# Optimization experiments

Hardware: AMD Instinct MI355X
Metric: run time of the kernel (lower is better)

The kernel has to match this reference:

```python
import jax, jax.numpy as jnp
import numpy as np

H = 56; W = 56; WS = 7; SHIFT = 3; C = 128; NH = 4; HD = C // NH
N = WS * WS; NW = (H // WS) * (W // WS); B = 64; HID = 4 * C
ALPHA = (1, 2, 4, 8); SCALE = HD ** -0.5


def _rel_index_np():
    coords = np.stack(np.meshgrid(np.arange(WS), np.arange(WS), indexing="ij"))
    cf = coords.reshape(2, -1)
    rel = (cf[:, :, None] - cf[:, None, :]).transpose(1, 2, 0).copy()
    rel[:, :, 0] += WS - 1
    rel[:, :, 1] += WS - 1
    rel[:, :, 0] *= 2 * WS - 1
    return rel.sum(-1).astype(np.int32)  # (N, N)


def _attn_mask_np():
    img = np.zeros((1, H, W, 1), np.float32)
    cnt = 0
    sl = (slice(0, -WS), slice(-WS, -SHIFT), slice(-SHIFT, None))
    for hs in sl:
        for ws in sl:
            img[:, hs, ws, :] = cnt
            cnt += 1
    mw = img.reshape(1, H // WS, WS, W // WS, WS, 1).transpose(0, 1, 3, 2, 4, 5).reshape(-1, N)
    am = mw[:, None, :] - mw[:, :, None]
    return np.where(am != 0, -100.0, 0.0).astype(np.float32)  # (NW, N, N)


def setup_inputs() -> dict:
    key = jax.random.key(0)
    ks = jax.random.split(key, 8)
    p = lambda k, shp, s=0.02: jax.random.normal(k, shp, jnp.float32) * s
    return {
        "x": jax.random.normal(ks[0], (B, H * W, C), jnp.float32),
        "gumbel_weights": jax.nn.softmax(jax.random.normal(ks[1], (4,), jnp.float32)),
        "norm1_w": jnp.ones((C,), jnp.float32), "norm1_b": jnp.zeros((C,), jnp.float32),
        "qkv_w": p(ks[2], (3 * C, C)), "qkv_b": jnp.zeros((3 * C,), jnp.float32),
        "rel_bias_table": p(ks[3], ((2 * WS - 1) ** 2, NH)),
        "proj_w": p(ks[4], (C, C)), "proj_b": jnp.zeros((C,), jnp.float32),
        "attn_mask": jnp.asarray(_attn_mask_np()),
        "norm2_w": jnp.ones((C,), jnp.float32), "norm2_b": jnp.zeros((C,), jnp.float32),
        "fc1_w": p(ks[5], (HID, C)), "fc1_b": jnp.zeros((HID,), jnp.float32),
        "fc2_w": p(ks[6], (C, HID)), "fc2_b": jnp.zeros((C,), jnp.float32),
        "rel_index": jnp.asarray(_rel_index_np()),
    }


def _ln(x, w, b, eps=1e-5):
    mu = x.mean(-1, keepdims=True)
    var = ((x - mu) ** 2).mean(-1, keepdims=True)
    return (x - mu) * jax.lax.rsqrt(var + eps) * w + b


def _win_part(x):  # (B,H,W,C) -> (B*NW, N, C)
    b = x.shape[0]
    x = x.reshape(b, H // WS, WS, W // WS, WS, C).transpose(0, 1, 3, 2, 4, 5)
    return x.reshape(-1, N, C)


def _win_rev(w, b):  # (b*NW, N, C) -> (b,H,W,C)
    x = w.reshape(b, H // WS, W // WS, WS, WS, C).transpose(0, 1, 3, 2, 4, 5)
    return x.reshape(b, H, W, C)


def _window_attn(xw, qkv_w, qkv_b, bias, mask, proj_w, proj_b):
    b = xw.shape[0]
    qkv = (xw @ qkv_w.T + qkv_b).reshape(b, N, 3, NH, HD).transpose(2, 0, 3, 1, 4)
    q, k, v = qkv[0] * SCALE, qkv[1], qkv[2]  # (b,NH,N,HD)
    a = jnp.einsum("bhnd,bhmd->bhnm", q, k) + bias[None]
    a = (a.reshape(b // NW, NW, NH, N, N) + mask[None, :, None]).reshape(b, NH, N, N)
    a = jax.nn.softmax(a, axis=-1)
    o = jnp.einsum("bhnm,bhmd->bhnd", a, v).transpose(0, 2, 1, 3).reshape(b, N, C)
    return o @ proj_w.T + proj_b


def _forward(x, gw, n1w, n1b, qkv_w, qkv_b, rbt, pw, pb, am, n2w, n2b, f1w, f1b, f2w, f2b, rel_index):
    shortcut = x
    xs = _ln(x, n1w, n1b).reshape(B, H, W, C)
    xs = jnp.roll(xs, (-SHIFT, -SHIFT), axis=(1, 2))  # cyclic shift
    xw = _win_part(xs)  # (B*NW, N, C)
    bias = rbt[rel_index.reshape(-1)].reshape(N, N, NH).transpose(2, 0, 1)  # (NH,N,N)
    half = xw.shape[0] // 2
    xw_l, xw_s = xw[:half], xw[half:]
    # large half: full-width window attention
    y_l = _window_attn(xw_l, qkv_w, qkv_b, bias, am, pw, pb)
    # small half: gumbel-gated slimmable branches (zero channels beyond C//alpha in/out)
    ch = jnp.arange(C)
    y_s = jnp.zeros_like(xw_s)
    for i, a in enumerate(ALPHA):
        if a > NH:
            continue
        cm = (ch < C // a).astype(xw.dtype)
        yb = _window_attn(xw_s * cm, qkv_w, qkv_b, bias, am, pw, pb) * cm
        y_s = y_s + yb * gw[i]
    attn_out = jnp.concatenate([y_l, y_s], axis=0)
    xr = _win_rev(attn_out, B)
    xr = jnp.roll(xr, (SHIFT, SHIFT), axis=(1, 2)).reshape(B, H * W, C)
    x = shortcut + xr
    # MLP with gumbel-gated slimmable small half (matches Mlp.forward)
    xn = _ln(x, n2w, n2b)
    xn_l, xn_s = xn[: B // 2], xn[B // 2 :]
    m_l = jax.nn.gelu(xn_l @ f1w.T + f1b, approximate=False) @ f2w.T + f2b
    m_s = jnp.zeros_like(xn_s)
    for i, a in enumerate(ALPHA):
        if a > NH:
            continue
        cm = (ch < C // a).astype(xn.dtype)
        yb = (jax.nn.gelu((xn_s * cm) @ f1w.T + f1b, approximate=False) @ f2w.T + f2b) * cm
        m_s = m_s + yb * gw[i]
    mlp_out = jnp.concatenate([m_l, m_s], axis=0)
    return x + mlp_out


def reference(x, gumbel_weights, norm1_w, norm1_b, qkv_w, qkv_b, rel_bias_table, proj_w, proj_b, attn_mask, norm2_w, norm2_b, fc1_w, fc1_b, fc2_w, fc2_b, rel_index):
    return _forward(x, gumbel_weights, norm1_w, norm1_b, qkv_w, qkv_b, rel_bias_table, proj_w, proj_b, attn_mask, norm2_w, norm2_b, fc1_w, fc1_b, fc2_w, fc2_b, rel_index)
```

## Files before the change

kernel.cpp:

```cpp
#include <hip/hip_runtime.h>
#include <hip/hip_bf16.h>

#define SHIFT_ 3
#define SCALE_ 0.17677669529663687f
#define NTOK   200704
#define NWIN   4096

typedef short v8s __attribute__((ext_vector_type(8)));
typedef float v4f __attribute__((ext_vector_type(4)));
#define MFMA16(a, b, c) __builtin_amdgcn_mfma_f32_16x16x32_bf16(a, b, c, 0, 0, 0)

static __device__ __forceinline__ unsigned short f2bf(float f) {
    union { float f; unsigned int u; } v; v.f = f;
    unsigned int u = v.u;
    unsigned int r = u + 0x7FFFu + ((u >> 16) & 1u);
    return (unsigned short)(r >> 16);
}
static __device__ __forceinline__ float wsum(float v) {
    #pragma unroll
    for (int o = 32; o; o >>= 1) v += __shfl_xor(v, o);
    return v;
}
static __device__ __forceinline__ float gelu_f(float v) {
    float w = v * v;
    float t = v * fmaf(w, 0.07135481283f, 1.595769122f);
    float e = __expf(-t);
    return v * __builtin_amdgcn_rcpf(1.f + e);
}

#define WS_COMB  67108864
#define WS_WQKV  71303168
#define WS_WPROJ 71401472
#define WS_F1W   71434240
#define WS_F2W   71565312

__global__ __launch_bounds__(256) void k_prep(
    const float* __restrict__ amask, const float* __restrict__ rbt,
    const int* __restrict__ relidx,
    const float* __restrict__ qkvw, const float* __restrict__ projw,
    const float* __restrict__ f1w, const float* __restrict__ f2w,
    float* __restrict__ comb, unsigned short* __restrict__ wqkv,
    unsigned short* __restrict__ wproj, unsigned short* __restrict__ f1wb,
    unsigned short* __restrict__ f2wb, unsigned short* __restrict__ xw) {
    int idx = blockIdx.x * 256 + threadIdx.x;
    if (idx < 1048576) {
        int wpos = idx >> 14;
        int h = (idx >> 12) & 3;
        int i = (idx >> 6) & 63;
        int j = idx & 63;
        float v;
        if (j >= 49) v = -1e30f;
        else if (i >= 49) v = 0.f;
        else v = amask[wpos * 2401 + i * 49 + j] + rbt[relidx[i * 49 + j] * 4 + h];
        comb[idx] = v;
    } else if (idx < 1048576 + 49152) {
        int k = idx - 1048576; wqkv[k] = f2bf(qkvw[k]);
    } else if (idx < 1048576 + 49152 + 16384) {
        int k = idx - (1048576 + 49152); wproj[k] = f2bf(projw[k]);
    } else if (idx < 1048576 + 49152 + 16384 + 65536) {
        int k = idx - (1048576 + 49152 + 16384); f1wb[k] = f2bf(f1w[k]);
    } else if (idx < 1048576 + 49152 + 16384 + 65536 + 65536) {
        int k = idx - (1048576 + 49152 + 16384 + 65536); f2wb[k] = f2bf(f2w[k]);
    } else {
        int k = idx - 1245184;
        if (k < 983040) {
            int win = k / 240, r = k - win * 240;
            uint4 z = make_uint4(0u, 0u, 0u, 0u);
            *(uint4*)((char*)xw + (size_t)win * 16384 + 12544 + (size_t)r * 16) = z;
        }
    }
}

__global__ __launch_bounds__(256) void k_ln1(const float* __restrict__ x,
                                             const float* __restrict__ nw,
                                             const float* __restrict__ nb,
                                             unsigned short* __restrict__ xw) {
    int tok  = blockIdx.x * 4 + (threadIdx.x >> 6);
    int lane = threadIdx.x & 63;
    int win = tok / 49, t = tok - win * 49;
    int bb = win >> 6, wh = (win >> 3) & 7, ww = win & 7;
    int i = t / 7, j = t - i * 7;
    int h  = wh * 7 + i + SHIFT_; if (h  >= 56) h  -= 56;
    int w2 = ww * 7 + j + SHIFT_; if (w2 >= 56) w2 -= 56;
    const float* src = x + ((size_t)bb * 3136 + h * 56 + w2) * 128;
    float v0 = src[lane], v1 = src[lane + 64];
    float mu = wsum(v0 + v1) * (1.f / 128.f);
    float d0 = v0 - mu, d1 = v1 - mu;
    float var = wsum(d0 * d0 + d1 * d1) * (1.f / 128.f);
    float inv = rsqrtf(var + 1e-5f);
    unsigned short* dst = xw + (size_t)win * 8192 + t * 128;
    dst[lane]      = f2bf(d0 * inv * nw[lane]      + nb[lane]);
    dst[lane + 64] = f2bf(d1 * inv * nw[lane + 64] + nb[lane + 64]);
}

__global__ __launch_bounds__(256) void k_ln2(const float* __restrict__ x2,
                                             const float* __restrict__ nw,
                                             const float* __restrict__ nb,
                                             unsigned short* __restrict__ xn) {
    int tok  = blockIdx.x * 4 + (threadIdx.x >> 6);
    int lane = threadIdx.x & 63;
    const float* src = x2 + (size_t)tok * 128;
    float v0 = src[lane], v1 = src[lane + 64];
    float mu = wsum(v0 + v1) * (1.f / 128.f);
    float d0 = v0 - mu, d1 = v1 - mu;
    float var = wsum(d0 * d0 + d1 * d1) * (1.f / 128.f);
    float inv = rsqrtf(var + 1e-5f);
    unsigned short* dst = xn + (size_t)tok * 128;
    dst[lane]      = f2bf(d0 * inv * nw[lane]      + nb[lane]);
    dst[lane + 64] = f2bf(d1 * inv * nw[lane + 64] + nb[lane + 64]);
}

template<int KA>
__device__ __forceinline__ void attn_pass(
    const v8s (&ax)[4][4],
    const unsigned short* __restrict__ wqkv, const float* __restrict__ qkvb,
    const float* __restrict__ comb,
    const unsigned short* __restrict__ wproj, const float* __restrict__ pbias,
    float wgt, int wpos, int wv, int li, int lg,
    unsigned short* __restrict__ s_q, unsigned short* __restrict__ s_k,
    unsigned short* __restrict__ s_v, unsigned short* __restrict__ pw_,
    v4f (&yacc)[2][4])
{
    const v4f z4 = {0.f, 0.f, 0.f, 0.f};
    constexpr int Ca = KA * 32;

    #pragma unroll 2
    for (int nt = 0; nt < 6; nt++) {
        const int ntg = wv * 6 + nt, o0 = ntg * 16;
        v4f acc[4] = {z4, z4, z4, z4};
        #pragma unroll
        for (int k = 0; k < KA; k++) {
            v8s b = *(const v8s*)(wqkv + (o0 + li) * 128 + k * 32 + lg * 8);
            #pragma unroll
            for (int m = 0; m < 4; m++) acc[m] = MFMA16(ax[m][k], b, acc[m]);
        }
        float bo = qkvb[o0 + li];
        if (ntg < 16) {
            unsigned short* dst = (ntg < 8) ? s_q : s_k;
            const int oc = (ntg < 8) ? o0 : o0 - 128;
            const float scl = (ntg < 8) ? SCALE_ : 1.f;
            #pragma unroll
            for (int m = 0; m < 4; m++)
                #pragma unroll
                for (int r = 0; r < 4; r++)
                    dst[(m * 16 + lg * 4 + r) * 136 + oc + li] =
                        f2bf((acc[m][r] + bo) * scl);
        } else {
            const int d = (ntg - 16) * 16 + li;
            #pragma unroll
            for (int m = 0; m < 4; m++) {
                int t0_ = m * 16 + lg * 4;
                unsigned int p0 = (unsigned int)f2bf(acc[m][0] + bo) |
                                  ((unsigned int)f2bf(acc[m][1] + bo) << 16);
                unsigned int p1 = (unsigned int)f2bf(acc[m][2] + bo) |
                                  ((unsigned int)f2bf(acc[m][3] + bo) << 16);
                *(unsigned int*)(s_v + d * 72 + t0_)     = p0;
                *(unsigned int*)(s_v + d * 72 + t0_ + 2) = p1;
            }
        }
    }
    __syncthreads();

    v4f oacc[8];
    #pragma unroll
    for (int i = 0; i < 8; i++) oacc[i] = z4;
    #pragma unroll
    for (int h = 0; h < 4; h++) {
        v8s aq = *(const v8s*)(s_q + (wv * 16 + li) * 136 + h * 32 + lg * 8);
        v4f sc[4];
        #pragma unroll
        for (int ntj = 0; ntj < 4; ntj++) {
            v8s bk = *(const v8s*)(s_k + (ntj * 16 + li) * 136 + h * 32 + lg * 8);
            sc[ntj] = MFMA16(aq, bk, z4);
        }
        const float* cb = comb + ((size_t)(wpos * 4 + h) << 12) + (wv * 16 + lg * 4) * 64;
        #pragma unroll
        for (int r = 0; r < 4; r++) {
            float vmax = -3.0e38f, e[4];
            #pragma unroll
            for (int ntj = 0; ntj < 4; ntj++) {
                float v_ = sc[ntj][r] + cb[r * 64 + ntj * 16 + li];
                sc[ntj][r] = v_;
                vmax = fmaxf(vmax, v_);
            }
            #pragma unroll
            for (int o_ = 1; o_ < 16; o_ <<= 1) vmax = fmaxf(vmax, __shfl_xor(vmax, o_));
            float ssum = 0.f;
            #pragma unroll
            for (int ntj = 0; ntj < 4; ntj++) {
                e[ntj] = __expf(sc[ntj][r] - vmax);
                ssum += e[ntj];
            }
            #pragma unroll
            for (int o_ = 1; o_ < 16; o_ <<= 1) ssum += __shfl_xor(ssum, o_);
            float inv = __builtin_amdgcn_rcpf(ssum);
            #pragma unroll
            for (int ntj = 0; ntj < 4; ntj++)
                pw_[(lg * 4 + r) * 72 + ntj * 16 + li] = f2bf(e[ntj] * inv);
        }
        #pragma unroll
        for (int k0 = 0; k0 < 2; k0++) {
            v8s ap = *(const v8s*)(pw_ + li * 72 + k0 * 32 + lg * 8);
            #pragma unroll
            for (int dn = 0; dn < 2; dn++) {
                v8s bv = *(const v8s*)(s_v + (h * 32 + dn * 16 + li) * 72 + k0 * 32 + lg * 8);
                oacc[h * 2 + dn] = MFMA16(ap, bv, oacc[h * 2 + dn]);
            }
        }
    }
    __syncthreads();

    unsigned short* s_o = s_k;
    #pragma unroll
    for (int ot = 0; ot < 8; ot++)
        #pragma unroll
        for (int r = 0; r < 4; r++)
            s_o[(wv * 16 + lg * 4 + r) * 136 + ot * 16 + li] = f2bf(oacc[ot][r]);
    __syncthreads();

    if (KA == 4 || wv * 16 < Ca) {
        v8s ao[4][4];
        #pragma unroll
        for (int m = 0; m < 4; m++)
            #pragma unroll
            for (int k = 0; k < 4; k++)
                ao[m][k] = *(const v8s*)(s_o + (m * 16 + li) * 136 + k * 32 + lg * 8);
        #pragma unroll
        for (int nt = 0; nt < 2; nt++) {
            const int co0 = (nt * 4 + wv) * 16;
            if (nt == 0 || Ca == 128) {
                if (co0 < Ca) {
                    v4f pacc[4] = {z4, z4, z4, z4};
                    #pragma unroll
                    for (int k = 0; k < 4; k++) {
                        v8s b = *(const v8s*)(wproj + (co0 + li) * 128 + k * 32 + lg * 8);
                        #pragma unroll
                        for (int m = 0; m < 4; m++) pacc[m] = MFMA16(ao[m][k], b, pacc[m]);
                    }
                    float bo = pbias[co0 + li];
                    #pragma unroll
                    for (int m = 0; m < 4; m++)
                        #pragma unroll
                        for (int r = 0; r < 4; r++)
                            yacc[nt][m][r] += wgt * (pacc[m][r] + bo);
                }
            }
        }
    }
    __syncthreads();
}

__global__ __launch_bounds__(256, 2) void k_attn(
    const unsigned short* __restrict__ xw,
    const unsigned short* __restrict__ wqkv, const float* __restrict__ qkvb,
    const float* __restrict__ comb,
    const unsigned short* __restrict__ wproj, const float* __restrict__ pbias,
    const float* __restrict__ gw,
    const float* __restrict__ x, float* __restrict__ out) {

    __shared__ unsigned short sm[31232];
    unsigned short* s_q = sm;
    unsigned short* s_k = sm + 8704;
    unsigned short* s_v = sm + 17408;
    unsigned short* s_p = sm + 26624;

    const int tid = threadIdx.x, wv = tid >> 6, lane = tid & 63;
    const int li = lane & 15, lg = lane >> 4;
    const int w = blockIdx.x;
    const int wpos = w & 63;
    const bool sp = (w >= 2048);
    const unsigned short* xwin = xw + (size_t)w * 8192;
    unsigned short* pw_ = s_p + wv * 1152;

    const v4f z4 = {0.f, 0.f, 0.f, 0.f};
    v4f yacc[2][4];
    #pragma unroll
    for (int n = 0; n < 2; n++)
        #pragma unroll
        for (int m = 0; m < 4; m++) yacc[n][m] = z4;

    v8s ax[4][4];
    #pragma unroll
    for (int m = 0; m < 4; m++)
        #pragma unroll
        for (int k = 0; k < 4; k++)
            ax[m][k] = *(const v8s*)(xwin + (m * 16 + li) * 128 + k * 32 + lg * 8);

    if (sp) {
        attn_pass<4>(ax, wqkv, qkvb, comb, wproj, pbias, gw[0], wpos, wv, li, lg,
                     s_q, s_k, s_v, pw_, yacc);
        attn_pass<2>(ax, wqkv, qkvb, comb, wproj, pbias, gw[1], wpos, wv, li, lg,
                     s_q, s_k, s_v, pw_, yacc);
        attn_pass<1>(ax, wqkv, qkvb, comb, wproj, pbias, gw[2], wpos, wv, li, lg,
                     s_q, s_k, s_v, pw_, yacc);
    } else {
        attn_pass<4>(ax, wqkv, qkvb, comb, wproj, pbias, 1.f, wpos, wv, li, lg,
                     s_q, s_k, s_v, pw_, yacc);
    }

    float* s_y = (float*)sm;
    #pragma unroll
    for (int m = 0; m < 4; m++)
        #pragma unroll
        for (int r = 0; r < 4; r++) {
            int t = m * 16 + lg * 4 + r;
            #pragma unroll
            for (int nt = 0; nt < 2; nt++)
                s_y[t * 132 + (nt * 4 + wv) * 16 + li] = yacc[nt][m][r];
        }
    __syncthreads();

    const int bb = w >> 6, wh = (w >> 3) & 7, ww = w & 7;
    const int rgrp = tid >> 5;
    const int col  = (tid & 31) * 4;
    #pragma unroll
    for (int it = 0; it < 7; it++) {
        int t = it * 8 + rgrp;
        if (t < 49) {
            int ti = t / 7, tj = t - ti * 7;
            int h2 = wh * 7 + ti + SHIFT_; if (h2 >= 56) h2 -= 56;
            int w2 = ww * 7 + tj + SHIFT_; if (w2 >= 56) w2 -= 56;
            size_t base = ((size_t)bb * 3136 + h2 * 56 + w2) * 128 + col;
            v4f xv = *(const v4f*)(x + base);
            v4f yv = *(const v4f*)(s_y + t * 132 + col);
            *(v4f*)(out + base) = xv + yv;
        }
    }
}

template<int KA>
__device__ __forceinline__ void mlp_pass(
    const v8s (&ax)[2][4],
    const unsigned short* __restrict__ f1wb, const float* __restrict__ f1b,
    const unsigned short* __restrict__ f2wb, const float* __restrict__ f2b,
    float wgt, int wv, int li, int lg,
    unsigned short* __restrict__ s_h, v4f (&yacc)[2][2])
{
    const v4f z4 = {0.f, 0.f, 0.f, 0.f};
    constexpr int Ca = KA * 32;

    #pragma unroll 4
    for (int nt = 0; nt < 8; nt++) {
        const int o0 = wv * 128 + nt * 16;
        v4f acc[2] = {z4, z4};
        #pragma unroll
        for (int k = 0; k < KA; k++) {
            v8s b = *(const v8s*)(f1wb + (o0 + li) * 128 + k * 32 + lg * 8);
            acc[0] = MFMA16(ax[0][k], b, acc[0]);
            acc[1] = MFMA16(ax[1][k], b, acc[1]);
        }
        float bo = f1b[o0 + li];
        #pragma unroll
        for (int m = 0; m < 2; m++)
            #pragma unroll
            for (int r = 0; r < 4; r++) {
                float v_ = gelu_f(acc[m][r] + bo);
                s_h[(m * 16 + lg * 4 + r) * 520 + o0 + li] = f2bf(v_);
            }
    }
    __syncthreads();

    if (KA == 4) {
        const int c0 = wv * 16, c1 = 64 + wv * 16;
        v4f acc2[2][2] = {{z4, z4}, {z4, z4}};
        #pragma unroll
        for (int k = 0; k < 16; k++) {
            v8s a0 = *(const v8s*)(s_h + li * 520 + k * 32 + lg * 8);
            v8s a1 = *(const v8s*)(s_h + (16 + li) * 520 + k * 32 + lg * 8);
            v8s b0 = *(const v8s*)(f2wb + (c0 + li) * 512 + k * 32 + lg * 8);
            v8s b1 = *(const v8s*)(f2wb + (c1 + li) * 512 + k * 32 + lg * 8);
            acc2[0][0] = MFMA16(a0, b0, acc2[0][0]);
            acc2[0][1] = MFMA16(a1, b0, acc2[0][1]);
            acc2[1][0] = MFMA16(a0, b1, acc2[1][0]);
            acc2[1][1] = MFMA16(a1, b1, acc2[1][1]);
        }
        float bo0 = f2b[c0 + li], bo1 = f2b[c1 + li];
        #pragma unroll
        for (int m = 0; m < 2; m++)
            #pragma unroll
            for (int r = 0; r < 4; r++) {
                yacc[0][m][r] += wgt * (acc2[0][m][r] + bo0);
                yacc[1][m][r] += wgt * (acc2[1][m][r] + bo1);
            }
    } else if (KA == 2 || wv < 2) {
        const int c0 = wv * 16;
        v4f acc2[2] = {z4, z4};
        #pragma unroll
        for (int k = 0; k < 16; k++) {
            v8s a0 = *(const v8s*)(s_h + li * 520 + k * 32 + lg * 8);
            v8s a1 = *(const v8s*)(s_h + (16 + li) * 520 + k * 32 + lg * 8);
            v8s b0 = *(const v8s*)(f2wb + (c0 + li) * 512 + k * 32 + lg * 8);
            acc2[0] = MFMA16(a0, b0, acc2[0]);
            acc2[1] = MFMA16(a1, b0, acc2[1]);
        }
        float bo0 = f2b[c0 + li];
        #pragma unroll
        for (int m = 0; m < 2; m++)
            #pragma unroll
            for (int r = 0; r < 4; r++)
                yacc[0][m][r] += wgt * (acc2[m][r] + bo0);
    }
}

__global__ __launch_bounds__(256, 3) void k_mlp(
    const unsigned short* __restrict__ xn,
    const unsigned short* __restrict__ f1wb, const float* __restrict__ f1b,
    const unsigned short* __restrict__ f2wb, const float* __restrict__ f2b,
    const float* __restrict__ gw, float* __restrict__ out) {

    __shared__ unsigned short s_h[32 * 520];

    const int tid = threadIdx.x, wv = tid >> 6, lane = tid & 63;
    const int li = lane & 15, lg = lane >> 4;
    const int t0 = blockIdx.x * 32;
    const bool sp = (t0 >= 100352);

    const v4f z4 = {0.f, 0.f, 0.f, 0.f};
    v4f yacc[2][2];
    #pragma unroll
    for (int n = 0; n < 2; n++)
        #pragma unroll
        for (int m = 0; m < 2; m++) yacc[n][m] = z4;

    v8s ax[2][4];
    #pragma unroll
    for (int m = 0; m < 2; m++)
        #pragma unroll
        for (int k = 0; k < 4; k++)
            ax[m][k] = *(const v8s*)(xn + (size_t)(t0 + m * 16 + li) * 128 + k * 32 + lg * 8);

    if (sp) {
        mlp_pass<4>(ax, f1wb, f1b, f2wb, f2b, gw[0], wv, li, lg, s_h, yacc);
        __syncthreads();
        mlp_pass<2>(ax, f1wb, f1b, f2wb, f2b, gw[1], wv, li, lg, s_h, yacc);
        __syncthreads();
        mlp_pass<1>(ax, f1wb, f1b, f2wb, f2b, gw[2], wv, li, lg, s_h, yacc);
    } else {
        mlp_pass<4>(ax, f1wb, f1b, f2wb, f2b, 1.f, wv, li, lg, s_h, yacc);
    }

    __syncthreads();
    float* s_y = (float*)s_h;
    #pragma unroll
    for (int m = 0; m < 2; m++)
        #pragma unroll
        for (int r = 0; r < 4; r++) {
            int t = m * 16 + lg * 4 + r;
            #pragma unroll
            for (int nt = 0; nt < 2; nt++)
                s_y[t * 132 + (nt * 4 + wv) * 16 + li] = yacc[nt][m][r];
        }
    __syncthreads();

    const int rgrp = tid >> 5;
    const int col  = (tid & 31) * 4;
    #pragma unroll
    for (int it = 0; it < 4; it++) {
        int t = it * 8 + rgrp;
        size_t base = (size_t)(t0 + t) * 128 + col;
        v4f ov = *(const v4f*)(out + base);
        v4f yv = *(const v4f*)(s_y + t * 132 + col);
        *(v4f*)(out + base) = ov + yv;
    }
}

extern "C" void kernel_launch(void* const* d_in, const int* in_sizes, int n_in,
                              void* d_out, int out_size, void* d_ws, size_t ws_size,
                              hipStream_t stream) {
    const float* x      = (const float*)d_in[0];
    const float* gw     = (const float*)d_in[1];
    const float* n1w    = (const float*)d_in[2];
    const float* n1b    = (const float*)d_in[3];
    const float* qkvw   = (const float*)d_in[4];
    const float* qkvb   = (const float*)d_in[5];
    const float* rbt    = (const float*)d_in[6];
    const float* pw     = (const float*)d_in[7];
    const float* pb     = (const float*)d_in[8];
    const float* amask  = (const float*)d_in[9];
    const float* n2w    = (const float*)d_in[10];
    const float* n2b    = (const float*)d_in[11];
    const float* f1w    = (const float*)d_in[12];
    const float* f1b    = (const float*)d_in[13];
    const float* f2w    = (const float*)d_in[14];
    const float* f2b    = (const float*)d_in[15];
    const int*   relidx = (const int*)d_in[16];
    float* out = (float*)d_out;

    unsigned short* xw    = (unsigned short*)d_ws;
    float*          comb  = (float*)((char*)d_ws + WS_COMB);
    unsigned short* wqkv  = (unsigned short*)((char*)d_ws + WS_WQKV);
    unsigned short* wproj = (unsigned short*)((char*)d_ws + WS_WPROJ);
    unsigned short* f1wb  = (unsigned short*)((char*)d_ws + WS_F1W);
    unsigned short* f2wb  = (unsigned short*)((char*)d_ws + WS_F2W);
    unsigned short* xn    = (unsigned short*)d_ws;

    hipLaunchKernelGGL(k_prep, dim3(8704), dim3(256), 0, stream,
                       amask, rbt, relidx, qkvw, pw, f1w, f2w,
                       comb, wqkv, wproj, f1wb, f2wb, xw);
    hipLaunchKernelGGL(k_ln1, dim3(NTOK / 4), dim3(256), 0, stream, x, n1w, n1b, xw);
    hipLaunchKernelGGL(k_attn, dim3(NWIN), dim3(256), 0, stream,
                       xw, wqkv, qkvb, comb, wproj, pb, gw, x, out);
    hipLaunchKernelGGL(k_ln2, dim3(NTOK / 4), dim3(256), 0, stream, out, n2w, n2b, xn);
    hipLaunchKernelGGL(k_mlp, dim3(NTOK / 32), dim3(256), 0, stream,
                       xn, f1wb, f1b, f2wb, f2b, gw, out);
}
```

Measured before the change: 778.5 us.

## Fuse LayerNorm1 and LayerNorm2 into the window attention kernel

Computes LN1 inside the attention kernel, gathering the shifted window tokens from x and normalizing them into shared memory, which removes the separate LN1 kernel and the bf16 window buffer round trip through global memory. LN2 is computed in the attention epilogue from the residual sum and written as bf16 for the MLP kernel, which removes the LN2 kernel and its reread of out. The prep kernel no longer zero-pads the window buffer. Variance now uses the single-pass E[x^2]-mu^2 form, which is slightly less numerically robust, and the attention kernel takes on extra loads, shuffles and barriers.

```diff
diff --git a/kernel.cpp b/kernel.cpp
--- a/kernel.cpp
+++ b/kernel.cpp
@@ -15,11 +15,6 @@
     unsigned int u = v.u;
     unsigned int r = u + 0x7FFFu + ((u >> 16) & 1u);
     return (unsigned short)(r >> 16);
-}
-static __device__ __forceinline__ float wsum(float v) {
-    #pragma unroll
-    for (int o = 32; o; o >>= 1) v += __shfl_xor(v, o);
-    return v;
 }
 static __device__ __forceinline__ float gelu_f(float v) {
     float w = v * v;
@@ -41,7 +36,7 @@
     const float* __restrict__ f1w, const float* __restrict__ f2w,
     float* __restrict__ comb, unsigned short* __restrict__ wqkv,
     unsigned short* __restrict__ wproj, unsigned short* __restrict__ f1wb,
-    unsigned short* __restrict__ f2wb, unsigned short* __restrict__ xw) {
+    unsigned short* __restrict__ f2wb) {
     int idx = blockIdx.x * 256 + threadIdx.x;
     if (idx < 1048576) {
         int wpos = idx >> 14;
@@ -61,53 +56,7 @@
         int k = idx - (1048576 + 49152 + 16384); f1wb[k] = f2bf(f1w[k]);
     } else if (idx < 1048576 + 49152 + 16384 + 65536 + 65536) {
         int k = idx - (1048576 + 49152 + 16384 + 65536); f2wb[k] = f2bf(f2w[k]);
-    } else {
-        int k = idx - 1245184;
-        if (k < 983040) {
-            int win = k / 240, r = k - win * 240;
-            uint4 z = make_uint4(0u, 0u, 0u, 0u);
-            *(uint4*)((char*)xw + (size_t)win * 16384 + 12544 + (size_t)r * 16) = z;
-        }
-    }
-}
-
-__global__ __launch_bounds__(256) void k_ln1(const float* __restrict__ x,
-                                             const float* __restrict__ nw,
-                                             const float* __restrict__ nb,
-                                             unsigned short* __restrict__ xw) {
-    int tok  = blockIdx.x * 4 + (threadIdx.x >> 6);
-    int lane = threadIdx.x & 63;
-    int win = tok / 49, t = tok - win * 49;
-    int bb = win >> 6, wh = (win >> 3) & 7, ww = win & 7;
-    int i = t / 7, j = t - i * 7;
-    int h  = wh * 7 + i + SHIFT_; if (h  >= 56) h  -= 56;
-    int w2 = ww * 7 + j + SHIFT_; if (w2 >= 56) w2 -= 56;
-    const float* src = x + ((size_t)bb * 3136 + h * 56 + w2) * 128;
-    float v0 = src[lane], v1 = src[lane + 64];
-    float mu = wsum(v0 + v1) * (1.f / 128.f);
-    float d0 = v0 - mu, d1 = v1 - mu;
-    float var = wsum(d0 * d0 + d1 * d1) * (1.f / 128.f);
-    float inv = rsqrtf(var + 1e-5f);
-    unsigned short* dst = xw + (size_t)win * 8192 + t * 128;
-    dst[lane]      = f2bf(d0 * inv * nw[lane]      + nb[lane]);
-    dst[lane + 64] = f2bf(d1 * inv * nw[lane + 64] + nb[lane + 64]);
-}
-
-__global__ __launch_bounds__(256) void k_ln2(const float* __restrict__ x2,
-                                             const float* __restrict__ nw,
-                                             const float* __restrict__ nb,
-                                             unsigned short* __restrict__ xn) {
-    int tok  = blockIdx.x * 4 + (threadIdx.x >> 6);
-    int lane = threadIdx.x & 63;
-    const float* src = x2 + (size_t)tok * 128;
-    float v0 = src[lane], v1 = src[lane + 64];
-    float mu = wsum(v0 + v1) * (1.f / 128.f);
-    float d0 = v0 - mu, d1 = v1 - mu;
-    float var = wsum(d0 * d0 + d1 * d1) * (1.f / 128.f);
-    float inv = rsqrtf(var + 1e-5f);
-    unsigned short* dst = xn + (size_t)tok * 128;
-    dst[lane]      = f2bf(d0 * inv * nw[lane]      + nb[lane]);
-    dst[lane + 64] = f2bf(d1 * inv * nw[lane + 64] + nb[lane + 64]);
+    }
 }
 
 template<int KA>
@@ -251,12 +200,14 @@
 }
 
 __global__ __launch_bounds__(256, 2) void k_attn(
-    const unsigned short* __restrict__ xw,
     const unsigned short* __restrict__ wqkv, const float* __restrict__ qkvb,
     const float* __restrict__ comb,
     const unsigned short* __restrict__ wproj, const float* __restrict__ pbias,
     const float* __restrict__ gw,
-    const float* __restrict__ x, float* __restrict__ out) {
+    const float* __restrict__ x,
+    const float* __restrict__ n1w, const float* __restrict__ n1b,
+    const float* __restrict__ n2w, const float* __restrict__ n2b,
+    float* __restrict__ out, unsigned short* __restrict__ xn) {
 
     __shared__ unsigned short sm[31232];
     unsigned short* s_q = sm;
@@ -269,8 +220,57 @@
     const int w = blockIdx.x;
     const int wpos = w & 63;
     const bool sp = (w >= 2048);
-    const unsigned short* xwin = xw + (size_t)w * 8192;
+    const int bb = w >> 6, wh = (w >> 3) & 7, ww = w & 7;
     unsigned short* pw_ = s_p + wv * 1152;
+
+    {
+        unsigned short* s_x = s_q;
+        float4 g0 = *(const float4*)(n1w + li * 8);
+        float4 g1 = *(const float4*)(n1w + li * 8 + 4);
+        float4 c0 = *(const float4*)(n1b + li * 8);
+        float4 c1 = *(const float4*)(n1b + li * 8 + 4);
+        #pragma unroll
+        for (int bq = 0; bq < 4; bq++) {
+            int t = wv * 16 + bq * 4 + lg;
+            float4 xa = {0.f, 0.f, 0.f, 0.f}, xb = {0.f, 0.f, 0.f, 0.f};
+            if (t < 49) {
+                int ti = t / 7, tj = t - ti * 7;
+                int h2 = wh * 7 + ti + SHIFT_; if (h2 >= 56) h2 -= 56;
+                int w2 = ww * 7 + tj + SHIFT_; if (w2 >= 56) w2 -= 56;
+                const float* src = x + ((size_t)bb * 3136 + h2 * 56 + w2) * 128 + li * 8;
+                xa = *(const float4*)src;
+                xb = *(const float4*)(src + 4);
+            }
+            float s  = xa.x + xa.y + xa.z + xa.w + xb.x + xb.y + xb.z + xb.w;
+            float sq = xa.x*xa.x + xa.y*xa.y + xa.z*xa.z + xa.w*xa.w
+                     + xb.x*xb.x + xb.y*xb.y + xb.z*xb.z + xb.w*xb.w;
+            #pragma unroll
+            for (int o_ = 1; o_ < 16; o_ <<= 1) {
+                s  += __shfl_xor(s, o_);
+                sq += __shfl_xor(sq, o_);
+            }
+            float mu  = s * (1.f / 128.f);
+            float var = sq * (1.f / 128.f) - mu * mu;
+            float inv = rsqrtf(var + 1e-5f);
+            uint4 P = make_uint4(0u, 0u, 0u, 0u);
+            if (t < 49) {
+                float y0 = (xa.x - mu) * inv * g0.x + c0.x;
+                float y1 = (xa.y - mu) * inv * g0.y + c0.y;
+                float y2 = (xa.z - mu) * inv * g0.z + c0.z;
+                float y3 = (xa.w - mu) * inv * g0.w + c0.w;
+                float y4 = (xb.x - mu) * inv * g1.x + c1.x;
+                float y5 = (xb.y - mu) * inv * g1.y + c1.y;
+                float y6 = (xb.z - mu) * inv * g1.z + c1.z;
+                float y7 = (xb.w - mu) * inv * g1.w + c1.w;
+                P.x = (unsigned int)f2bf(y0) | ((unsigned int)f2bf(y1) << 16);
+                P.y = (unsigned int)f2bf(y2) | ((unsigned int)f2bf(y3) << 16);
+                P.z = (unsigned int)f2bf(y4) | ((unsigned int)f2bf(y5) << 16);
+                P.w = (unsigned int)f2bf(y6) | ((unsigned int)f2bf(y7) << 16);
+            }
+            *(uint4*)(s_x + (size_t)t * 136 + li * 8) = P;
+        }
+    }
+    __syncthreads();
 
     const v4f z4 = {0.f, 0.f, 0.f, 0.f};
     v4f yacc[2][4];
@@ -284,7 +284,8 @@
     for (int m = 0; m < 4; m++)
         #pragma unroll
         for (int k = 0; k < 4; k++)
-            ax[m][k] = *(const v8s*)(xwin + (m * 16 + li) * 128 + k * 32 + lg * 8);
+            ax[m][k] = *(const v8s*)(s_q + (m * 16 + li) * 136 + k * 32 + lg * 8);
+    __syncthreads();
 
     if (sp) {
         attn_pass<4>(ax, wqkv, qkvb, comb, wproj, pbias, gw[0], wpos, wv, li, lg,
@@ -310,9 +311,10 @@
         }
     __syncthreads();
 
-    const int bb = w >> 6, wh = (w >> 3) & 7, ww = w & 7;
     const int rgrp = tid >> 5;
     const int col  = (tid & 31) * 4;
+    float4 g2 = *(const float4*)(n2w + col);
+    float4 c2 = *(const float4*)(n2b + col);
     #pragma unroll
     for (int it = 0; it < 7; it++) {
         int t = it * 8 + rgrp;
@@ -320,10 +322,28 @@
             int ti = t / 7, tj = t - ti * 7;
             int h2 = wh * 7 + ti + SHIFT_; if (h2 >= 56) h2 -= 56;
             int w2 = ww * 7 + tj + SHIFT_; if (w2 >= 56) w2 -= 56;
-            size_t base = ((size_t)bb * 3136 + h2 * 56 + w2) * 128 + col;
+            size_t tok  = (size_t)bb * 3136 + h2 * 56 + w2;
+            size_t base = tok * 128 + col;
             v4f xv = *(const v4f*)(x + base);
             v4f yv = *(const v4f*)(s_y + t * 132 + col);
-            *(v4f*)(out + base) = xv + yv;
+            v4f ov = xv + yv;
+            *(v4f*)(out + base) = ov;
+            float s  = ov[0] + ov[1] + ov[2] + ov[3];
+            float sq = ov[0]*ov[0] + ov[1]*ov[1] + ov[2]*ov[2] + ov[3]*ov[3];
+            #pragma unroll
+            for (int o_ = 1; o_ < 32; o_ <<= 1) {
+                s  += __shfl_xor(s, o_);
+                sq += __shfl_xor(sq, o_);
+            }
+            float mu  = s * (1.f / 128.f);
+            float var = sq * (1.f / 128.f) - mu * mu;
+            float inv = rsqrtf(var + 1e-5f);
+            unsigned int q0 = (unsigned int)f2bf((ov[0] - mu) * inv * g2.x + c2.x) |
+                              ((unsigned int)f2bf((ov[1] - mu) * inv * g2.y + c2.y) << 16);
+            unsigned int q1 = (unsigned int)f2bf((ov[2] - mu) * inv * g2.z + c2.z) |
+                              ((unsigned int)f2bf((ov[3] - mu) * inv * g2.w + c2.w) << 16);
+            uint2 Q; Q.x = q0; Q.y = q1;
+            *(uint2*)(xn + tok * 128 + col) = Q;
         }
     }
 }
@@ -486,21 +506,19 @@
     const int*   relidx = (const int*)d_in[16];
     float* out = (float*)d_out;
 
-    unsigned short* xw    = (unsigned short*)d_ws;
+    unsigned short* xn    = (unsigned short*)d_ws;
     float*          comb  = (float*)((char*)d_ws + WS_COMB);
     unsigned short* wqkv  = (unsigned short*)((char*)d_ws + WS_WQKV);
     unsigned short* wproj = (unsigned short*)((char*)d_ws + WS_WPROJ);
     unsigned short* f1wb  = (unsigned short*)((char*)d_ws + WS_F1W);
     unsigned short* f2wb  = (unsigned short*)((char*)d_ws + WS_F2W);
-    unsigned short* xn    = (unsigned short*)d_ws;
-
-    hipLaunchKernelGGL(k_prep, dim3(8704), dim3(256), 0, stream,
+
+    hipLaunchKernelGGL(k_prep, dim3(4864), dim3(256), 0, stream,
                        amask, rbt, relidx, qkvw, pw, f1w, f2w,
-                       comb, wqkv, wproj, f1wb, f2wb, xw);
-    hipLaunchKernelGGL(k_ln1, dim3(NTOK / 4), dim3(256), 0, stream, x, n1w, n1b, xw);
+                       comb, wqkv, wproj, f1wb, f2wb);
     hipLaunchKernelGGL(k_attn, dim3(NWIN), dim3(256), 0, stream,
-                       xw, wqkv, qkvb, comb, wproj, pb, gw, x, out);
-    hipLaunchKernelGGL(k_ln2, dim3(NTOK / 4), dim3(256), 0, stream, out, n2w, n2b, xn);
+                       wqkv, qkvb, comb, wproj, pb, gw, x,
+                       n1w, n1b, n2w, n2b, out, xn);
     hipLaunchKernelGGL(k_mlp, dim3(NTOK / 32), dim3(256), 0, stream,
                        xn, f1wb, f1b, f2wb, f2b, gw, out);
 }
```

New measurement: 726.3 us. 1.07x faster.
